# Kernel optimization log

Hardware: AMD Instinct MI355X
Metric: run time of the kernel (lower is better)

## Reference

```python
import jax, jax.numpy as jnp
import numpy as np

N = 100000      # nodes
E = 1600000     # edges (avg degree 16)
B = 64          # graphs in batch
DIN = 128
HID = (256, 128, 64)
EPS = 1e-5


def _gcn(x, W, b, src, dst, n):
    # GCNConv: symmetric normalization with self-loops (already appended to src/dst)
    h = x @ W                                                   # [N, out]
    deg = jax.ops.segment_sum(jnp.ones_like(dst, dtype=h.dtype), dst, num_segments=n)
    dinv = jnp.where(deg > 0, jax.lax.rsqrt(jnp.maximum(deg, 1.0)), 0.0)
    norm = dinv[src] * dinv[dst]                                # [E+N]
    msg = h[src] * norm[:, None]                                # gather + scale
    return jax.ops.segment_sum(msg, dst, num_segments=n) + b    # scatter-add


def _bn(x, g, b):
    # BatchNorm1d over nodes (batch statistics, deterministic)
    mu = x.mean(0)
    var = x.var(0)
    return (x - mu) * jax.lax.rsqrt(var + EPS) * g + b


def setup_inputs():
    key = jax.random.key(0)
    ks = jax.random.split(key, 32)
    inp = {}
    inp["x"] = jax.random.normal(ks[0], (N, DIN), jnp.float32)
    inp["edge_index"] = jax.random.randint(ks[1], (2, E), 0, N, jnp.int32)
    inp["batch"] = jnp.sort(jax.random.randint(ks[2], (N,), 0, B, jnp.int32))
    dims = [DIN] + list(HID)
    for i in range(3):
        inp[f"W{i}"] = jax.random.normal(ks[3 + 4 * i], (dims[i], dims[i + 1]), jnp.float32) / np.sqrt(dims[i]).astype(np.float32)
        inp[f"b{i}"] = jnp.zeros((dims[i + 1],), jnp.float32)
        inp[f"g{i}"] = jnp.ones((dims[i + 1],), jnp.float32)
        inp[f"be{i}"] = jnp.zeros((dims[i + 1],), jnp.float32)
    d = HID[-1]
    inp["ln_g"] = jnp.ones((d,), jnp.float32)
    inp["ln_b"] = jnp.zeros((d,), jnp.float32)
    inp["att"] = jax.random.normal(ks[15], (d, 1), jnp.float32)
    mdims = [d, d // 2, d // 4, 2]
    for i in range(3):
        inp[f"M{i}W"] = jax.random.normal(ks[16 + 2 * i], (mdims[i], mdims[i + 1]), jnp.float32) / np.sqrt(mdims[i]).astype(np.float32)
        inp[f"M{i}b"] = jnp.zeros((mdims[i + 1],), jnp.float32)
    return inp


def reference(x, edge_index, batch, W0, b0, g0, be0, W1, b1, g1, be1, W2, b2, g2, be2,
              ln_g, ln_b, att, M0W, M0b, M1W, M1b, M2W, M2b):
    n = x.shape[0]
    loop = jnp.arange(n, dtype=edge_index.dtype)
    src = jnp.concatenate([edge_index[0], loop])
    dst = jnp.concatenate([edge_index[1], loop])
    for (W, b, g, be) in ((W0, b0, g0, be0), (W1, b1, g1, be1), (W2, b2, g2, be2)):
        x = jax.nn.relu(_bn(_gcn(x, W, b, src, dst, n), g, be))
    # LayerNorm over features
    mu = x.mean(-1, keepdims=True)
    var = x.var(-1, keepdims=True)
    x = (x - mu) * jax.lax.rsqrt(var + EPS) * ln_g + ln_b
    # global attention weights (softmax over ALL nodes, as in original code)
    aw = jax.nn.softmax(jnp.tanh(x @ att), axis=0)   # [N, 1]
    x = x * aw
    # global mean pool per graph
    s = jax.ops.segment_sum(x, batch, num_segments=B)
    cnt = jax.ops.segment_sum(jnp.ones((n, 1), x.dtype), batch, num_segments=B)
    pooled = s / jnp.maximum(cnt, 1.0)               # [B, 64]
    h = jax.nn.relu(pooled @ M0W + M0b)
    h = jax.nn.relu(h @ M1W + M1b)
    return h @ M2W + M2b                             # [B, 2]
```

## Files before the change

### kernel.cpp

```cpp
#include <hip/hip_runtime.h>
#include <hip/hip_bf16.h>
#include <cstdint>
#include <cstddef>

typedef float    f32x4  __attribute__((ext_vector_type(4)));
typedef _Float16 f16x4  __attribute__((ext_vector_type(4)));
typedef _Float16 f16x8  __attribute__((ext_vector_type(8)));

#define BN_G1 1024

__global__ void k_hist(const int* __restrict__ dst, int* __restrict__ deg, int E,
                       unsigned long long M,
                       const int* __restrict__ batch, int* __restrict__ cnt, int n){
  __shared__ int h[64];
  if(threadIdx.x<64) h[threadIdx.x]=0;
  __syncthreads();
  int f   = blockIdx.x & 7;
  int cid = blockIdx.x >> 3;
  int nch = gridDim.x >> 3;
  for(int i = cid*blockDim.x + threadIdx.x; i < E; i += nch*blockDim.x){
    int d = dst[i];
    int xf = (int)(((unsigned long long)(unsigned)d * M) >> 40);
    if(xf == f) atomicAdd(&deg[d], 1);
  }
  for(int i = blockIdx.x*blockDim.x + threadIdx.x; i < n; i += gridDim.x*blockDim.x)
    atomicAdd(&h[batch[i]], 1);
  __syncthreads();
  if(threadIdx.x<64 && h[threadIdx.x]) atomicAdd(&cnt[threadIdx.x], h[threadIdx.x]);
}

__global__ void k_scan1(const int* __restrict__ deg, int* __restrict__ bsum, int n){
  __shared__ int s[256];
  int base = blockIdx.x*1024 + threadIdx.x*4;
  int acc=0;
  #pragma unroll
  for(int j=0;j<4;j++){ int i=base+j; if(i<n) acc+=deg[i]; }
  s[threadIdx.x]=acc; __syncthreads();
  for(int off=128;off>0;off>>=1){
    if(threadIdx.x<off) s[threadIdx.x]+=s[threadIdx.x+off];
    __syncthreads();
  }
  if(threadIdx.x==0) bsum[blockIdx.x]=s[0];
}

__global__ void k_scan2(int* __restrict__ bsum, int nblk, int* __restrict__ rowptr, int n){
  __shared__ int s[128];
  int t=threadIdx.x;
  int v = (t<nblk)? bsum[t] : 0;
  s[t]=v; __syncthreads();
  for(int off=1; off<128; off<<=1){
    int a = (t>=off)? s[t-off] : 0;
    __syncthreads();
    s[t]+=a;
    __syncthreads();
  }
  if(t<nblk) bsum[t]=s[t]-v;
  if(t==127) rowptr[n]=s[127];
}

__global__ void k_scan3(const int* __restrict__ deg, const int* __restrict__ bsum,
                        int* __restrict__ rowptr, int* __restrict__ cursor, int n){
  __shared__ int s[256];
  int base = blockIdx.x*1024 + threadIdx.x*4;
  int v[4]; int acc=0;
  #pragma unroll
  for(int j=0;j<4;j++){ int i=base+j; v[j]=(i<n)?deg[i]:0; acc+=v[j]; }
  s[threadIdx.x]=acc; __syncthreads();
  for(int off=1; off<256; off<<=1){
    int a = (threadIdx.x>=off)? s[threadIdx.x-off] : 0;
    __syncthreads();
    s[threadIdx.x]+=a;
    __syncthreads();
  }
  int excl = s[threadIdx.x]-acc + bsum[blockIdx.x];
  #pragma unroll
  for(int j=0;j<4;j++){
    int i=base+j;
    if(i<n){ rowptr[i]=excl; cursor[i]=excl; excl+=v[j]; }
  }
}

__global__ void k_csr_fill(const int* __restrict__ src, const int* __restrict__ dst,
                           int* __restrict__ cursor, int* __restrict__ adj, int E,
                           unsigned long long M){
  int f   = blockIdx.x & 7;
  int cid = blockIdx.x >> 3;
  int nch = gridDim.x >> 3;
  for(int i = cid*blockDim.x + threadIdx.x; i < E; i += nch*blockDim.x){
    int d = dst[i];
    int xf = (int)(((unsigned long long)(unsigned)d * M) >> 40);
    if(xf == f){
      int p = atomicAdd(&cursor[d], 1);
      adj[p] = src[i];
    }
  }
}


__global__ void k_prep_w3(const float* __restrict__ W0, const float* __restrict__ W1,
                          const float* __restrict__ W2,
                          _Float16* __restrict__ Wh0, _Float16* __restrict__ Wl0,
                          _Float16* __restrict__ Wh1, _Float16* __restrict__ Wl1,
                          _Float16* __restrict__ Wh2, _Float16* __restrict__ Wl2){
  int i = blockIdx.x*256 + threadIdx.x;
  const float* W; _Float16 *Wh, *Wl; int K, F, idx;
  if(i < 32768){        W=W0; Wh=Wh0; Wl=Wl0; K=128; F=256; idx=i; }
  else if(i < 65536){   W=W1; Wh=Wh1; Wl=Wl1; K=256; F=128; idx=i-32768; }
  else if(i < 73728){   W=W2; Wh=Wh2; Wl=Wl2; K=128; F=64;  idx=i-65536; }
  else return;
  int k = idx / F, f = idx % F;
  float a = W[idx];
  _Float16 h = (_Float16)a;
  Wh[(size_t)f*K + k] = h;
  Wl[(size_t)f*K + k] = (_Float16)(a - (float)h);
}

__global__ void k_prep_x(const float* __restrict__ x, const int* __restrict__ deg,
                         float* __restrict__ dinv, _Float16* __restrict__ x16, int n){
  int tid = blockIdx.x*256 + threadIdx.x;
  int node = tid >> 5;
  if(node>=n) return;
  int c4 = tid & 31;
  float d = rsqrtf((float)(deg[node]+1));
  if(c4==0) dinv[node] = d;
  size_t idx = ((size_t)node<<5) + c4;
  float4 v = ((const float4*)x)[idx];
  f16x4 o;
  o[0]=(_Float16)(v.x*d); o[1]=(_Float16)(v.y*d); o[2]=(_Float16)(v.z*d); o[3]=(_Float16)(v.w*d);
  ((f16x4*)x16)[idx] = o;
}

__global__ void k_agg16(const _Float16* __restrict__ zs, const int* __restrict__ rowptr,
                        const int* __restrict__ adj, const float* __restrict__ dinv,
                        const float* __restrict__ bias, _Float16* __restrict__ out,
                        int n, int lg8){
  int tid = blockIdx.x*blockDim.x + threadIdx.x;
  int node = tid >> lg8;
  if(node>=n) return;
  int c8 = tid & ((1<<lg8)-1);
  const f16x8* z8 = (const f16x8*)zs;
  size_t rb = ((size_t)node<<lg8) + c8;
  f16x8 self = z8[rb];
  float a0[8], a1[8], a2[8], a3[8];
  #pragma unroll
  for(int j=0;j<8;j++){ a0[j]=(float)self[j]; a1[j]=0.f; a2[j]=0.f; a3[j]=0.f; }
  int e = rowptr[node], end = rowptr[node+1];
  for(; e+3<end; e+=4){
    int s0=adj[e], s1=adj[e+1], s2=adj[e+2], s3=adj[e+3];
    f16x8 v0 = z8[((size_t)s0<<lg8)+c8];
    f16x8 v1 = z8[((size_t)s1<<lg8)+c8];
    f16x8 v2 = z8[((size_t)s2<<lg8)+c8];
    f16x8 v3 = z8[((size_t)s3<<lg8)+c8];
    #pragma unroll
    for(int j=0;j<8;j++){
      a0[j]+=(float)v0[j]; a1[j]+=(float)v1[j];
      a2[j]+=(float)v2[j]; a3[j]+=(float)v3[j];
    }
  }
  for(; e<end; e++){
    f16x8 v0 = z8[((size_t)adj[e]<<lg8)+c8];
    #pragma unroll
    for(int j=0;j<8;j++) a0[j]+=(float)v0[j];
  }
  float di = dinv[node];
  f16x8 o;
  #pragma unroll
  for(int j=0;j<8;j++){
    float r = ((a0[j]+a1[j])+(a2[j]+a3[j]))*di;
    if(bias) r += bias[(c8<<3)+j];
    o[j] = (_Float16)r;
  }
  ((f16x8*)out)[rb] = o;
}

template<int K, int F, bool BN, bool BIAS, bool RSC>
__global__ __launch_bounds__(256,2) void k_gemm_mfma(const _Float16* __restrict__ A,
    const _Float16* __restrict__ Bh, const _Float16* __restrict__ Bl,
    const float* __restrict__ sc, const float* __restrict__ sh,
    const float* __restrict__ bias, const float* __restrict__ rsc,
    _Float16* __restrict__ C, int n){
  constexpr int NF = F/16;
  __shared__ uint4 sBh[F*4];
  __shared__ uint4 sBl[F*4];
  const int l   = threadIdx.x & 63;
  const int w   = threadIdx.x >> 6;
  const int rlo = l & 15;
  const int khi = l >> 4;
  const int row0 = blockIdx.x*128 + w*32;

  f32x4 acc[2][NF];
  #pragma unroll
  for(int i=0;i<2;i++)
    #pragma unroll
    for(int j=0;j<NF;j++) acc[i][j] = (f32x4){0.f,0.f,0.f,0.f};

  const size_t e0 = (size_t)min(row0 + rlo,      n-1) * K + khi*8;
  const size_t e1 = (size_t)min(row0 + 16 + rlo, n-1) * K + khi*8;

  f16x8 c0 = *(const f16x8*)(A + e0);
  f16x8 c1 = *(const f16x8*)(A + e1);
  f16x8 n0v, n1v;

  #pragma unroll 1
  for(int k0=0; k0<K; k0+=32){
    if(k0+32 < K){
      n0v = *(const f16x8*)(A + e0 + k0 + 32);
      n1v = *(const f16x8*)(A + e1 + k0 + 32);
    }
    __syncthreads();
    #pragma unroll
    for(int j=0;j<F/64;j++){
      int i  = threadIdx.x + j*256;
      int f  = i >> 2;
      int k8 = i & 3;
      int g  = ((f>>4)<<6) + (k8<<4) + (f&15);
      size_t goff = (size_t)f*K + k0 + (k8<<3);
      sBh[g] = *(const uint4*)(Bh + goff);
      sBl[g] = *(const uint4*)(Bl + goff);
    }
    f16x8 a0, a1;
    if(BN){
      float scr[8], shr[8];
      float4 s0 = *(const float4*)(sc + k0 + khi*8);
      float4 s1 = *(const float4*)(sc + k0 + khi*8 + 4);
      float4 t0 = *(const float4*)(sh + k0 + khi*8);
      float4 t1 = *(const float4*)(sh + k0 + khi*8 + 4);
      scr[0]=s0.x;scr[1]=s0.y;scr[2]=s0.z;scr[3]=s0.w;scr[4]=s1.x;scr[5]=s1.y;scr[6]=s1.z;scr[7]=s1.w;
      shr[0]=t0.x;shr[1]=t0.y;shr[2]=t0.z;shr[3]=t0.w;shr[4]=t1.x;shr[5]=t1.y;shr[6]=t1.z;shr[7]=t1.w;
      #pragma unroll
      for(int j=0;j<8;j++){
        a0[j] = (_Float16)fmaxf(fmaf((float)c0[j],scr[j],shr[j]),0.f);
        a1[j] = (_Float16)fmaxf(fmaf((float)c1[j],scr[j],shr[j]),0.f);
      }
    }else{
      a0 = c0; a1 = c1;
    }
    __syncthreads();
    #pragma unroll
    for(int cf=0; cf<NF; cf++){
      f16x8 bh = ((const f16x8*)sBh)[cf*64 + l];
      f16x8 bl = ((const f16x8*)sBl)[cf*64 + l];
      acc[0][cf] = __builtin_amdgcn_mfma_f32_16x16x32_f16(a0, bh, acc[0][cf], 0,0,0);
      acc[1][cf] = __builtin_amdgcn_mfma_f32_16x16x32_f16(a1, bh, acc[1][cf], 0,0,0);
      acc[0][cf] = __builtin_amdgcn_mfma_f32_16x16x32_f16(a0, bl, acc[0][cf], 0,0,0);
      acc[1][cf] = __builtin_amdgcn_mfma_f32_16x16x32_f16(a1, bl, acc[1][cf], 0,0,0);
    }
    c0=n0v; c1=n1v;
  }

  #pragma unroll
  for(int rf=0; rf<2; rf++){
    #pragma unroll
    for(int r=0; r<4; r++){
      int m = row0 + rf*16 + khi*4 + r;
      if(m < n){
        float rs = RSC ? rsc[m] : 1.f;
        #pragma unroll
        for(int cf=0; cf<NF; cf++){
          int col = rlo + 16*cf;
          float v = acc[rf][cf][r];
          if(BIAS) v += bias[col];
          v *= rs;
          C[(size_t)m*F + col] = (_Float16)v;
        }
      }
    }
  }
}

__global__ __launch_bounds__(256) void k_bn_stats16(const _Float16* __restrict__ h,
                            float* __restrict__ partials, int n, int lgF){
  const int F   = 1 << lgF;
  const int C8  = 1 << (lgF-3);
  const int c8  = threadIdx.x & (C8-1);
  const int sub = threadIdx.x >> (lgF-3);
  const int rpb = 256 >> (lgF-3);
  float s[8], s2[8];
  #pragma unroll
  for(int j=0;j<8;j++){ s[j]=0.f; s2[j]=0.f; }
  for(int row = blockIdx.x*rpb + sub; row < n; row += gridDim.x*rpb){
    f16x8 v = ((const f16x8*)h)[(size_t)row*C8 + c8];
    #pragma unroll
    for(int j=0;j<8;j++){ float f=(float)v[j]; s[j]+=f; s2[j]=fmaf(f,f,s2[j]); }
  }
  __shared__ float rs [256*9];
  __shared__ float rs2[256*9];
  #pragma unroll
  for(int j=0;j<8;j++){ rs[threadIdx.x*9+j]=s[j]; rs2[threadIdx.x*9+j]=s2[j]; }
  __syncthreads();
  for(int half = rpb>>1; half>=1; half>>=1){
    if(sub < half){
      int o = (threadIdx.x + half*C8)*9;
      #pragma unroll
      for(int j=0;j<8;j++){ rs[threadIdx.x*9+j]+=rs[o+j]; rs2[threadIdx.x*9+j]+=rs2[o+j]; }
    }
    __syncthreads();
  }
  if(sub==0){
    float* p = partials + (size_t)blockIdx.x*(2*F);
    #pragma unroll
    for(int j=0;j<8;j++){
      p[c8*8+j]     = rs [threadIdx.x*9+j];
      p[F + c8*8+j] = rs2[threadIdx.x*9+j];
    }
  }
}

__global__ void k_bn_fin2(const float* __restrict__ partials, int F,
                          const float* __restrict__ g, const float* __restrict__ be,
                          float* __restrict__ scale, float* __restrict__ shift, int n){
  int c = blockIdx.x*64 + threadIdx.x;
  float s=0.f, s2=0.f;
  #pragma unroll 8
  for(int b=0; b<BN_G1; b++){
    const float* p = partials + (size_t)b*2*F;
    s  += p[c];
    s2 += p[F + c];
  }
  float mu = s/(float)n;
  float var = s2/(float)n - mu*mu;
  float sc = g[c]*rsqrtf(var+1e-5f);
  scale[c] = sc;
  shift[c] = fmaf(-mu, sc, be[c]);
}

__global__ void k_ln_att(const _Float16* __restrict__ x, const float* __restrict__ bsc, const float* __restrict__ bsh,
                         const float* __restrict__ g, const float* __restrict__ b,
                         const float* __restrict__ att, float* __restrict__ lnx, float* __restrict__ wv,
                         float* __restrict__ Ssum, int n){
  int lane = threadIdx.x & 63;
  int wid = (blockIdx.x<<2) + (threadIdx.x>>6);
  float gl=g[lane], bl=b[lane], al=att[lane];
  float scl=bsc[lane], shl=bsh[lane];
  float wacc=0.f;
  for(int node=wid; node<n; node+=4096){
    float raw = (float)x[((size_t)node<<6)+lane];
    float v = fmaxf(fmaf(raw, scl, shl), 0.f);
    float s=v;
    #pragma unroll
    for(int o=32;o>0;o>>=1) s += __shfl_xor(s,o);
    float mu = s*0.015625f;
    float d = v-mu;
    float q = d*d;
    #pragma unroll
    for(int o=32;o>0;o>>=1) q += __shfl_xor(q,o);
    float ln = d*rsqrtf(q*0.015625f + 1e-5f)*gl + bl;
    lnx[((size_t)node<<6)+lane] = ln;
    float a = ln*al;
    #pragma unroll
    for(int o=32;o>0;o>>=1) a += __shfl_xor(a,o);
    float wgt = expf(tanhf(a));
    if(lane==0) wv[node]=wgt;
    wacc += wgt;
  }
  __shared__ float sred[4];
  if(lane==0) sred[threadIdx.x>>6]=wacc;
  __syncthreads();
  if(threadIdx.x==0) atomicAdd(Ssum, sred[0]+sred[1]+sred[2]+sred[3]);
}

__global__ void k_pool(const float* __restrict__ lnx, const float* __restrict__ wv,
                       const int* __restrict__ batch, float* __restrict__ psum, int n){
  int lane = threadIdx.x & 63;
  int wave = threadIdx.x >> 6;
  int start = blockIdx.x*512 + wave*128;
  if(start >= n) return;
  int end = min(start+128, n);
  int cur = batch[start];
  float acc = 0.f;
  for(int i=start;i<end;i++){
    int bb = batch[i];
    if(bb != cur){ atomicAdd(&psum[cur*64+lane], acc); acc=0.f; cur=bb; }
    acc = fmaf(lnx[(size_t)i*64+lane], wv[i], acc);
  }
  atomicAdd(&psum[cur*64+lane], acc);
}

__global__ void k_mlp(const float* __restrict__ psum, const int* __restrict__ cnt,
                      const float* __restrict__ Ssum,
                      const float* __restrict__ M0W, const float* __restrict__ M0b,
                      const float* __restrict__ M1W, const float* __restrict__ M1b,
                      const float* __restrict__ M2W, const float* __restrict__ M2b,
                      float* __restrict__ out){
  int b = threadIdx.x;
  float S = Ssum[0];
  int cb = cnt[b]; if(cb<1) cb=1;
  float inv = 1.f/(S*(float)cb);
  float p[64];
  #pragma unroll
  for(int f=0;f<64;f++) p[f] = psum[b*64+f]*inv;
  float h1[32];
  #pragma unroll
  for(int j=0;j<32;j++){
    float a=M0b[j];
    #pragma unroll
    for(int f=0;f<64;f++) a = fmaf(p[f], M0W[f*32+j], a);
    h1[j]=fmaxf(a,0.f);
  }
  float h2[16];
  #pragma unroll
  for(int j=0;j<16;j++){
    float a=M1b[j];
    #pragma unroll
    for(int f=0;f<32;f++) a = fmaf(h1[f], M1W[f*16+j], a);
    h2[j]=fmaxf(a,0.f);
  }
  #pragma unroll
  for(int j=0;j<2;j++){
    float a=M2b[j];
    #pragma unroll
    for(int f=0;f<16;f++) a = fmaf(h2[f], M2W[f*2+j], a);
    out[b*2+j]=a;
  }
}


extern "C" void kernel_launch(void* const* d_in, const int* in_sizes, int n_in,
                              void* d_out, int out_size, void* d_ws, size_t ws_size,
                              hipStream_t stream){
  const float* x   = (const float*)d_in[0];
  const int*   ei  = (const int*)d_in[1];
  const int* batch = (const int*)d_in[2];
  const float* W0=(const float*)d_in[3],  *b0=(const float*)d_in[4],  *g0=(const float*)d_in[5],  *be0=(const float*)d_in[6];
  const float* W1=(const float*)d_in[7],  *b1=(const float*)d_in[8],  *g1=(const float*)d_in[9],  *be1=(const float*)d_in[10];
  const float* W2=(const float*)d_in[11], *b2=(const float*)d_in[12], *g2=(const float*)d_in[13], *be2=(const float*)d_in[14];
  const float* ln_g=(const float*)d_in[15], *ln_b=(const float*)d_in[16], *att=(const float*)d_in[17];
  const float* M0W=(const float*)d_in[18], *M0b=(const float*)d_in[19];
  const float* M1W=(const float*)d_in[20], *M1b=(const float*)d_in[21];
  const float* M2W=(const float*)d_in[22], *M2b=(const float*)d_in[23];
  const int N = in_sizes[0]/128;
  const int E = in_sizes[1]/2;
  const int* srcv = ei;
  const int* dstv = ei + E;
  const unsigned long long Mdiv = ((8ULL<<40) + (unsigned long long)N - 1) / (unsigned long long)N;

  char* base = (char*)d_ws;
  size_t off = 0;
  auto alloc = [&](size_t bytes)->char*{ char* p = base+off; off = (off+bytes+255)&~(size_t)255; return p; };
  int*   deg    = (int*)  alloc((size_t)N*4);
  int*   cnt    = (int*)  alloc(64*4);
  float* psum   = (float*)alloc(64*64*4);
  float* Ssum   = (float*)alloc(4);
  size_t zero_bytes = off;
  float* dinv   = (float*)alloc((size_t)N*4);
  int*   rowptr = (int*)  alloc(((size_t)N+1)*4);
  int*   cursor = (int*)  alloc((size_t)N*4);
  int*   bsum   = (int*)  alloc(128*4);
  float* bnsc   = (float*)alloc(3*256*4);
  float* bnsh   = (float*)alloc(3*256*4);
  float* partials = (float*)alloc((size_t)BN_G1*512*4);
  _Float16* Wh0 = (_Float16*)alloc((size_t)128*256*2);
  _Float16* Wl0 = (_Float16*)alloc((size_t)128*256*2);
  _Float16* Wh1 = (_Float16*)alloc((size_t)256*128*2);
  _Float16* Wl1 = (_Float16*)alloc((size_t)256*128*2);
  _Float16* Wh2 = (_Float16*)alloc((size_t)128*64*2);
  _Float16* Wl2 = (_Float16*)alloc((size_t)128*64*2);
  int*   adj    = (int*)  alloc((size_t)E*4);
  _Float16* x16 = (_Float16*)alloc((size_t)N*128*2);
  _Float16* R16 = (_Float16*)alloc((size_t)N*128*2);
  _Float16* P16 = (_Float16*)alloc((size_t)N*256*2);
  _Float16* Q16 = (_Float16*)alloc((size_t)N*128*2);
  _Float16* O16 = (_Float16*)alloc((size_t)N*64*2);
  float* LNX    = (float*)alloc((size_t)N*64*4);
  float* WV     = (float*)alloc((size_t)N*4);
  (void)ws_size; (void)n_in; (void)out_size;

  hipMemsetAsync(d_ws, 0, zero_bytes, stream);

  k_hist <<<2048,256,0,stream>>>(dstv, deg, E, Mdiv, batch, cnt, N);
  int nblk = (N+1023)/1024;
  k_scan1<<<nblk,256,0,stream>>>(deg, bsum, N);
  k_scan2<<<1,128,0,stream>>>(bsum, nblk, rowptr, N);
  k_scan3<<<nblk,256,0,stream>>>(deg, bsum, rowptr, cursor, N);
  k_csr_fill<<<2048,256,0,stream>>>(srcv, dstv, cursor, adj, E, Mdiv);
  k_prep_w3<<<288,256,0,stream>>>(W0,W1,W2, Wh0,Wl0, Wh1,Wl1, Wh2,Wl2);
  k_prep_x<<<(N*32+255)/256,256,0,stream>>>(x, deg, dinv, x16, N);

  const int gemm_grid = (N+127)/128;

  k_agg16<<<(N*16+255)/256,256,0,stream>>>(x16, rowptr, adj, dinv, nullptr, R16, N, 4);
  k_gemm_mfma<128,256,false,true,false><<<gemm_grid,256,0,stream>>>(R16, Wh0, Wl0, nullptr,nullptr, b0, nullptr, P16, N);
  k_bn_stats16<<<BN_G1,256,0,stream>>>(P16, partials, N, 8);
  k_bn_fin2<<<4,64,0,stream>>>(partials, 256, g0, be0, bnsc+0, bnsh+0, N);

  k_gemm_mfma<256,128,true,false,true><<<gemm_grid,256,0,stream>>>(P16, Wh1, Wl1, bnsc+0, bnsh+0, nullptr, dinv, Q16, N);
  k_agg16<<<(N*16+255)/256,256,0,stream>>>(Q16, rowptr, adj, dinv, b1, R16, N, 4);
  k_bn_stats16<<<BN_G1,256,0,stream>>>(R16, partials, N, 7);
  k_bn_fin2<<<2,64,0,stream>>>(partials, 128, g1, be1, bnsc+256, bnsh+256, N);

  k_gemm_mfma<128,64,true,false,true><<<gemm_grid,256,0,stream>>>(R16, Wh2, Wl2, bnsc+256, bnsh+256, nullptr, dinv, Q16, N);
  k_agg16<<<(N*8+255)/256,256,0,stream>>>(Q16, rowptr, adj, dinv, b2, O16, N, 3);
  k_bn_stats16<<<BN_G1,256,0,stream>>>(O16, partials, N, 6);
  k_bn_fin2<<<1,64,0,stream>>>(partials, 64, g2, be2, bnsc+512, bnsh+512, N);

  k_ln_att<<<1024,256,0,stream>>>(O16, bnsc+512, bnsh+512, ln_g, ln_b, att, LNX, WV, Ssum, N);
  k_pool  <<<(N+511)/512,256,0,stream>>>(LNX, WV, batch, psum, N);
  k_mlp   <<<1,64,0,stream>>>(psum, cnt, Ssum, M0W,M0b,M1W,M1b,M2W,M2b, (float*)d_out);
}
```

Measured before the change: 685.0 us.

## Fuse BatchNorm statistics into GEMM/aggregation epilogues and store LN output as fp16

Removes the standalone BN-stats kernels by computing per-column sum and sum-of-squares in the epilogues of the first GEMM and the second and third aggregation kernels. The per-block partials are then reduced in two levels (colsum slices, then finalize). This avoids rereading each large activation tensor just for statistics. It also stores the LayerNorm output in fp16 to halve pool traffic, and computes the attention weight with a clamped exp2-based tanh/exp. The costs are extra shared-memory reductions and barriers in the producer kernels, one extra small launch per layer, and slightly lower precision in the pooled features.

```diff
diff --git a/kernel.cpp b/kernel.cpp
--- a/kernel.cpp
+++ b/kernel.cpp
@@ -6,8 +6,6 @@
 typedef float    f32x4  __attribute__((ext_vector_type(4)));
 typedef _Float16 f16x4  __attribute__((ext_vector_type(4)));
 typedef _Float16 f16x8  __attribute__((ext_vector_type(8)));
-
-#define BN_G1 1024
 
 __global__ void k_hist(const int* __restrict__ dst, int* __restrict__ deg, int E,
                        unsigned long long M,
@@ -95,7 +93,6 @@
     }
   }
 }
-
 
 __global__ void k_prep_w3(const float* __restrict__ W0, const float* __restrict__ W1,
                           const float* __restrict__ W2,
@@ -130,55 +127,94 @@
   ((f16x4*)x16)[idx] = o;
 }
 
+template<bool STATS>
 __global__ void k_agg16(const _Float16* __restrict__ zs, const int* __restrict__ rowptr,
                         const int* __restrict__ adj, const float* __restrict__ dinv,
                         const float* __restrict__ bias, _Float16* __restrict__ out,
-                        int n, int lg8){
+                        float* __restrict__ partials, int n, int lg8){
   int tid = blockIdx.x*blockDim.x + threadIdx.x;
   int node = tid >> lg8;
-  if(node>=n) return;
-  int c8 = tid & ((1<<lg8)-1);
-  const f16x8* z8 = (const f16x8*)zs;
-  size_t rb = ((size_t)node<<lg8) + c8;
-  f16x8 self = z8[rb];
-  float a0[8], a1[8], a2[8], a3[8];
-  #pragma unroll
-  for(int j=0;j<8;j++){ a0[j]=(float)self[j]; a1[j]=0.f; a2[j]=0.f; a3[j]=0.f; }
-  int e = rowptr[node], end = rowptr[node+1];
-  for(; e+3<end; e+=4){
-    int s0=adj[e], s1=adj[e+1], s2=adj[e+2], s3=adj[e+3];
-    f16x8 v0 = z8[((size_t)s0<<lg8)+c8];
-    f16x8 v1 = z8[((size_t)s1<<lg8)+c8];
-    f16x8 v2 = z8[((size_t)s2<<lg8)+c8];
-    f16x8 v3 = z8[((size_t)s3<<lg8)+c8];
+  const int C8 = 1<<lg8;
+  int c8 = threadIdx.x & (C8-1);
+  bool valid = node < n;
+  if(!STATS && !valid) return;
+  float rr[8];
+  #pragma unroll
+  for(int j=0;j<8;j++) rr[j]=0.f;
+  if(valid){
+    const f16x8* z8 = (const f16x8*)zs;
+    size_t rb = ((size_t)node<<lg8) + c8;
+    f16x8 self = z8[rb];
+    float a0[8], a1[8], a2[8], a3[8];
+    #pragma unroll
+    for(int j=0;j<8;j++){ a0[j]=(float)self[j]; a1[j]=0.f; a2[j]=0.f; a3[j]=0.f; }
+    int e = rowptr[node], end = rowptr[node+1];
+    for(; e+3<end; e+=4){
+      int s0=adj[e], s1=adj[e+1], s2=adj[e+2], s3=adj[e+3];
+      f16x8 v0 = z8[((size_t)s0<<lg8)+c8];
+      f16x8 v1 = z8[((size_t)s1<<lg8)+c8];
+      f16x8 v2 = z8[((size_t)s2<<lg8)+c8];
+      f16x8 v3 = z8[((size_t)s3<<lg8)+c8];
+      #pragma unroll
+      for(int j=0;j<8;j++){
+        a0[j]+=(float)v0[j]; a1[j]+=(float)v1[j];
+        a2[j]+=(float)v2[j]; a3[j]+=(float)v3[j];
+      }
+    }
+    for(; e<end; e++){
+      f16x8 v0 = z8[((size_t)adj[e]<<lg8)+c8];
+      #pragma unroll
+      for(int j=0;j<8;j++) a0[j]+=(float)v0[j];
+    }
+    float di = dinv[node];
+    f16x8 o;
     #pragma unroll
     for(int j=0;j<8;j++){
-      a0[j]+=(float)v0[j]; a1[j]+=(float)v1[j];
-      a2[j]+=(float)v2[j]; a3[j]+=(float)v3[j];
-    }
-  }
-  for(; e<end; e++){
-    f16x8 v0 = z8[((size_t)adj[e]<<lg8)+c8];
-    #pragma unroll
-    for(int j=0;j<8;j++) a0[j]+=(float)v0[j];
-  }
-  float di = dinv[node];
-  f16x8 o;
-  #pragma unroll
-  for(int j=0;j<8;j++){
-    float r = ((a0[j]+a1[j])+(a2[j]+a3[j]))*di;
-    if(bias) r += bias[(c8<<3)+j];
-    o[j] = (_Float16)r;
-  }
-  ((f16x8*)out)[rb] = o;
-}
-
-template<int K, int F, bool BN, bool BIAS, bool RSC>
+      float r = ((a0[j]+a1[j])+(a2[j]+a3[j]))*di;
+      if(bias) r += bias[(c8<<3)+j];
+      rr[j]=r;
+      o[j] = (_Float16)r;
+    }
+    ((f16x8*)out)[rb] = o;
+  }
+  if constexpr(STATS){
+    __shared__ float rs [256*9];
+    __shared__ float rs2[256*9];
+    int sub = threadIdx.x >> lg8;
+    int npb = 256 >> lg8;
+    #pragma unroll
+    for(int j=0;j<8;j++){
+      float v = valid ? rr[j] : 0.f;
+      rs [threadIdx.x*9+j] = v;
+      rs2[threadIdx.x*9+j] = v*v;
+    }
+    __syncthreads();
+    for(int half = npb>>1; half>=1; half>>=1){
+      if(sub < half){
+        int o = (threadIdx.x + half*C8)*9;
+        #pragma unroll
+        for(int j=0;j<8;j++){ rs[threadIdx.x*9+j]+=rs[o+j]; rs2[threadIdx.x*9+j]+=rs2[o+j]; }
+      }
+      __syncthreads();
+    }
+    if(sub==0){
+      int F = 8<<lg8;
+      float* p = partials + (size_t)blockIdx.x*(2*F);
+      #pragma unroll
+      for(int j=0;j<8;j++){
+        p[c8*8+j]     = rs [threadIdx.x*9+j];
+        p[F + c8*8+j] = rs2[threadIdx.x*9+j];
+      }
+    }
+  }
+}
+
+template<int K, int F, bool BN, bool BIAS, bool RSC, bool STATS>
 __global__ __launch_bounds__(256,2) void k_gemm_mfma(const _Float16* __restrict__ A,
     const _Float16* __restrict__ Bh, const _Float16* __restrict__ Bl,
     const float* __restrict__ sc, const float* __restrict__ sh,
     const float* __restrict__ bias, const float* __restrict__ rsc,
-    _Float16* __restrict__ C, int n){
+    _Float16* __restrict__ C, float* __restrict__ partials, int n){
   constexpr int NF = F/16;
   __shared__ uint4 sBh[F*4];
   __shared__ uint4 sBl[F*4];
@@ -248,75 +284,73 @@
     c0=n0v; c1=n1v;
   }
 
+  float ts[NF], ts2[NF];
+  if constexpr(STATS){
+    #pragma unroll
+    for(int cf=0;cf<NF;cf++){ ts[cf]=0.f; ts2[cf]=0.f; }
+  }
   #pragma unroll
   for(int rf=0; rf<2; rf++){
     #pragma unroll
     for(int r=0; r<4; r++){
       int m = row0 + rf*16 + khi*4 + r;
       if(m < n){
-        float rs = RSC ? rsc[m] : 1.f;
+        float rscv = RSC ? rsc[m] : 1.f;
         #pragma unroll
         for(int cf=0; cf<NF; cf++){
           int col = rlo + 16*cf;
           float v = acc[rf][cf][r];
           if(BIAS) v += bias[col];
-          v *= rs;
+          v *= rscv;
           C[(size_t)m*F + col] = (_Float16)v;
+          if constexpr(STATS){ ts[cf]+=v; ts2[cf]=fmaf(v,v,ts2[cf]); }
         }
       }
     }
   }
-}
-
-__global__ __launch_bounds__(256) void k_bn_stats16(const _Float16* __restrict__ h,
-                            float* __restrict__ partials, int n, int lgF){
-  const int F   = 1 << lgF;
-  const int C8  = 1 << (lgF-3);
-  const int c8  = threadIdx.x & (C8-1);
-  const int sub = threadIdx.x >> (lgF-3);
-  const int rpb = 256 >> (lgF-3);
-  float s[8], s2[8];
-  #pragma unroll
-  for(int j=0;j<8;j++){ s[j]=0.f; s2[j]=0.f; }
-  for(int row = blockIdx.x*rpb + sub; row < n; row += gridDim.x*rpb){
-    f16x8 v = ((const f16x8*)h)[(size_t)row*C8 + c8];
-    #pragma unroll
-    for(int j=0;j<8;j++){ float f=(float)v[j]; s[j]+=f; s2[j]=fmaf(f,f,s2[j]); }
-  }
-  __shared__ float rs [256*9];
-  __shared__ float rs2[256*9];
-  #pragma unroll
-  for(int j=0;j<8;j++){ rs[threadIdx.x*9+j]=s[j]; rs2[threadIdx.x*9+j]=s2[j]; }
-  __syncthreads();
-  for(int half = rpb>>1; half>=1; half>>=1){
-    if(sub < half){
-      int o = (threadIdx.x + half*C8)*9;
+  if constexpr(STATS){
+    __shared__ float sstat[4][16][NF][2];
+    #pragma unroll
+    for(int cf=0;cf<NF;cf++){
+      ts [cf] += __shfl_xor(ts [cf],16); ts [cf] += __shfl_xor(ts [cf],32);
+      ts2[cf] += __shfl_xor(ts2[cf],16); ts2[cf] += __shfl_xor(ts2[cf],32);
+    }
+    if(khi==0){
       #pragma unroll
-      for(int j=0;j<8;j++){ rs[threadIdx.x*9+j]+=rs[o+j]; rs2[threadIdx.x*9+j]+=rs2[o+j]; }
-    }
-    __syncthreads();
-  }
-  if(sub==0){
-    float* p = partials + (size_t)blockIdx.x*(2*F);
-    #pragma unroll
-    for(int j=0;j<8;j++){
-      p[c8*8+j]     = rs [threadIdx.x*9+j];
-      p[F + c8*8+j] = rs2[threadIdx.x*9+j];
-    }
-  }
-}
-
-__global__ void k_bn_fin2(const float* __restrict__ partials, int F,
+      for(int cf=0;cf<NF;cf++){ sstat[w][rlo][cf][0]=ts[cf]; sstat[w][rlo][cf][1]=ts2[cf]; }
+    }
+    __syncthreads();
+    {
+      int rl = threadIdx.x & 15, cf = threadIdx.x >> 4;
+      float s_=0.f, s2_=0.f;
+      #pragma unroll
+      for(int ww=0; ww<4; ww++){ s_+=sstat[ww][rl][cf][0]; s2_+=sstat[ww][rl][cf][1]; }
+      int col = rl + 16*cf;
+      partials[(size_t)blockIdx.x*(2*F) + col]     = s_;
+      partials[(size_t)blockIdx.x*(2*F) + F + col] = s2_;
+    }
+  }
+}
+
+__global__ void k_colsum1(const float* __restrict__ partials, float* __restrict__ lvl1,
+                          int F2, int nblk){
+  int c = blockIdx.x*64 + threadIdx.x;
+  int slice = blockIdx.y;
+  int b0 = (int)(((long long)nblk *  slice   ) >> 6);
+  int b1 = (int)(((long long)nblk * (slice+1)) >> 6);
+  float s = 0.f;
+  for(int b=b0; b<b1; b++) s += partials[(size_t)b*F2 + c];
+  lvl1[slice*F2 + c] = s;
+}
+
+__global__ void k_bn_fin2(const float* __restrict__ lvl1, int F,
                           const float* __restrict__ g, const float* __restrict__ be,
                           float* __restrict__ scale, float* __restrict__ shift, int n){
   int c = blockIdx.x*64 + threadIdx.x;
+  int F2 = 2*F;
   float s=0.f, s2=0.f;
-  #pragma unroll 8
-  for(int b=0; b<BN_G1; b++){
-    const float* p = partials + (size_t)b*2*F;
-    s  += p[c];
-    s2 += p[F + c];
-  }
+  #pragma unroll
+  for(int k=0;k<64;k++){ s += lvl1[k*F2 + c]; s2 += lvl1[k*F2 + F + c]; }
   float mu = s/(float)n;
   float var = s2/(float)n - mu*mu;
   float sc = g[c]*rsqrtf(var+1e-5f);
@@ -324,34 +358,62 @@
   shift[c] = fmaf(-mu, sc, be[c]);
 }
 
+__device__ __forceinline__ float attw(float a){
+  float t = fminf(fmaxf(a,-15.f),15.f);
+  float u = exp2f(t*2.885390082f);
+  float th = (u-1.f)/(u+1.f);
+  return exp2f(th*1.442695041f);
+}
+
 __global__ void k_ln_att(const _Float16* __restrict__ x, const float* __restrict__ bsc, const float* __restrict__ bsh,
                          const float* __restrict__ g, const float* __restrict__ b,
-                         const float* __restrict__ att, float* __restrict__ lnx, float* __restrict__ wv,
+                         const float* __restrict__ att, _Float16* __restrict__ lnx, float* __restrict__ wv,
                          float* __restrict__ Ssum, int n){
   int lane = threadIdx.x & 63;
   int wid = (blockIdx.x<<2) + (threadIdx.x>>6);
   float gl=g[lane], bl=b[lane], al=att[lane];
   float scl=bsc[lane], shl=bsh[lane];
   float wacc=0.f;
-  for(int node=wid; node<n; node+=4096){
-    float raw = (float)x[((size_t)node<<6)+lane];
-    float v = fmaxf(fmaf(raw, scl, shl), 0.f);
-    float s=v;
-    #pragma unroll
-    for(int o=32;o>0;o>>=1) s += __shfl_xor(s,o);
-    float mu = s*0.015625f;
-    float d = v-mu;
-    float q = d*d;
-    #pragma unroll
-    for(int o=32;o>0;o>>=1) q += __shfl_xor(q,o);
-    float ln = d*rsqrtf(q*0.015625f + 1e-5f)*gl + bl;
-    lnx[((size_t)node<<6)+lane] = ln;
-    float a = ln*al;
-    #pragma unroll
-    for(int o=32;o>0;o>>=1) a += __shfl_xor(a,o);
-    float wgt = expf(tanhf(a));
-    if(lane==0) wv[node]=wgt;
-    wacc += wgt;
+  int node = wid;
+  for(; node+4096 < n; node += 8192){
+    int n1 = node + 4096;
+    float v0 = fmaxf(fmaf((float)x[((size_t)node<<6)+lane], scl, shl), 0.f);
+    float v1 = fmaxf(fmaf((float)x[((size_t)n1  <<6)+lane], scl, shl), 0.f);
+    float s0=v0, s1=v1;
+    #pragma unroll
+    for(int o=32;o>0;o>>=1){ s0+=__shfl_xor(s0,o); s1+=__shfl_xor(s1,o); }
+    float d0=v0-s0*0.015625f, d1=v1-s1*0.015625f;
+    float q0=d0*d0, q1=d1*d1;
+    #pragma unroll
+    for(int o=32;o>0;o>>=1){ q0+=__shfl_xor(q0,o); q1+=__shfl_xor(q1,o); }
+    float ln0 = d0*rsqrtf(q0*0.015625f+1e-5f)*gl+bl;
+    float ln1 = d1*rsqrtf(q1*0.015625f+1e-5f)*gl+bl;
+    lnx[((size_t)node<<6)+lane]=(_Float16)ln0;
+    lnx[((size_t)n1  <<6)+lane]=(_Float16)ln1;
+    float a0=ln0*al, a1=ln1*al;
+    #pragma unroll
+    for(int o=32;o>0;o>>=1){ a0+=__shfl_xor(a0,o); a1+=__shfl_xor(a1,o); }
+    float w0=attw(a0), w1=attw(a1);
+    if(lane==0){ wv[node]=w0; wv[n1]=w1; }
+    wacc += w0+w1;
+  }
+  for(; node<n; node+=4096){
+    float v0 = fmaxf(fmaf((float)x[((size_t)node<<6)+lane], scl, shl), 0.f);
+    float s0=v0;
+    #pragma unroll
+    for(int o=32;o>0;o>>=1) s0+=__shfl_xor(s0,o);
+    float d0=v0-s0*0.015625f;
+    float q0=d0*d0;
+    #pragma unroll
+    for(int o=32;o>0;o>>=1) q0+=__shfl_xor(q0,o);
+    float ln0 = d0*rsqrtf(q0*0.015625f+1e-5f)*gl+bl;
+    lnx[((size_t)node<<6)+lane]=(_Float16)ln0;
+    float a0=ln0*al;
+    #pragma unroll
+    for(int o=32;o>0;o>>=1) a0+=__shfl_xor(a0,o);
+    float w0=attw(a0);
+    if(lane==0) wv[node]=w0;
+    wacc += w0;
   }
   __shared__ float sred[4];
   if(lane==0) sred[threadIdx.x>>6]=wacc;
@@ -359,7 +421,7 @@
   if(threadIdx.x==0) atomicAdd(Ssum, sred[0]+sred[1]+sred[2]+sred[3]);
 }
 
-__global__ void k_pool(const float* __restrict__ lnx, const float* __restrict__ wv,
+__global__ void k_pool(const _Float16* __restrict__ lnx, const float* __restrict__ wv,
                        const int* __restrict__ batch, float* __restrict__ psum, int n){
   int lane = threadIdx.x & 63;
   int wave = threadIdx.x >> 6;
@@ -371,7 +433,7 @@
   for(int i=start;i<end;i++){
     int bb = batch[i];
     if(bb != cur){ atomicAdd(&psum[cur*64+lane], acc); acc=0.f; cur=bb; }
-    acc = fmaf(lnx[(size_t)i*64+lane], wv[i], acc);
+    acc = fmaf((float)lnx[(size_t)i*64+lane], wv[i], acc);
   }
   atomicAdd(&psum[cur*64+lane], acc);
 }
@@ -434,6 +496,10 @@
   const int* dstv = ei + E;
   const unsigned long long Mdiv = ((8ULL<<40) + (unsigned long long)N - 1) / (unsigned long long)N;
 
+  const int gemm_grid = (N+127)/128;
+  const int agg_grid1 = (N*16+255)/256;
+  const int agg_grid2 = (N*8+255)/256;
+
   char* base = (char*)d_ws;
   size_t off = 0;
   auto alloc = [&](size_t bytes)->char*{ char* p = base+off; off = (off+bytes+255)&~(size_t)255; return p; };
@@ -448,7 +514,8 @@
   int*   bsum   = (int*)  alloc(128*4);
   float* bnsc   = (float*)alloc(3*256*4);
   float* bnsh   = (float*)alloc(3*256*4);
-  float* partials = (float*)alloc((size_t)BN_G1*512*4);
+  float* partials = (float*)alloc((size_t)agg_grid1*256*4);
+  float* lvl1   = (float*)alloc((size_t)64*512*4);
   _Float16* Wh0 = (_Float16*)alloc((size_t)128*256*2);
   _Float16* Wl0 = (_Float16*)alloc((size_t)128*256*2);
   _Float16* Wh1 = (_Float16*)alloc((size_t)256*128*2);
@@ -461,7 +528,7 @@
   _Float16* P16 = (_Float16*)alloc((size_t)N*256*2);
   _Float16* Q16 = (_Float16*)alloc((size_t)N*128*2);
   _Float16* O16 = (_Float16*)alloc((size_t)N*64*2);
-  float* LNX    = (float*)alloc((size_t)N*64*4);
+  _Float16* LNX = (_Float16*)alloc((size_t)N*64*2);
   float* WV     = (float*)alloc((size_t)N*4);
   (void)ws_size; (void)n_in; (void)out_size;
 
@@ -476,22 +543,20 @@
   k_prep_w3<<<288,256,0,stream>>>(W0,W1,W2, Wh0,Wl0, Wh1,Wl1, Wh2,Wl2);
   k_prep_x<<<(N*32+255)/256,256,0,stream>>>(x, deg, dinv, x16, N);
 
-  const int gemm_grid = (N+127)/128;
-
-  k_agg16<<<(N*16+255)/256,256,0,stream>>>(x16, rowptr, adj, dinv, nullptr, R16, N, 4);
-  k_gemm_mfma<128,256,false,true,false><<<gemm_grid,256,0,stream>>>(R16, Wh0, Wl0, nullptr,nullptr, b0, nullptr, P16, N);
-  k_bn_stats16<<<BN_G1,256,0,stream>>>(P16, partials, N, 8);
-  k_bn_fin2<<<4,64,0,stream>>>(partials, 256, g0, be0, bnsc+0, bnsh+0, N);
-
-  k_gemm_mfma<256,128,true,false,true><<<gemm_grid,256,0,stream>>>(P16, Wh1, Wl1, bnsc+0, bnsh+0, nullptr, dinv, Q16, N);
-  k_agg16<<<(N*16+255)/256,256,0,stream>>>(Q16, rowptr, adj, dinv, b1, R16, N, 4);
-  k_bn_stats16<<<BN_G1,256,0,stream>>>(R16, partials, N, 7);
-  k_bn_fin2<<<2,64,0,stream>>>(partials, 128, g1, be1, bnsc+256, bnsh+256, N);
-
-  k_gemm_mfma<128,64,true,false,true><<<gemm_grid,256,0,stream>>>(R16, Wh2, Wl2, bnsc+256, bnsh+256, nullptr, dinv, Q16, N);
-  k_agg16<<<(N*8+255)/256,256,0,stream>>>(Q16, rowptr, adj, dinv, b2, O16, N, 3);
-  k_bn_stats16<<<BN_G1,256,0,stream>>>(O16, partials, N, 6);
-  k_bn_fin2<<<1,64,0,stream>>>(partials, 64, g2, be2, bnsc+512, bnsh+512, N);
+  k_agg16<false><<<agg_grid1,256,0,stream>>>(x16, rowptr, adj, dinv, nullptr, R16, nullptr, N, 4);
+  k_gemm_mfma<128,256,false,true,false,true><<<gemm_grid,256,0,stream>>>(R16, Wh0, Wl0, nullptr,nullptr, b0, nullptr, P16, partials, N);
+  k_colsum1<<<dim3(8,64),64,0,stream>>>(partials, lvl1, 512, gemm_grid);
+  k_bn_fin2<<<4,64,0,stream>>>(lvl1, 256, g0, be0, bnsc+0, bnsh+0, N);
+
+  k_gemm_mfma<256,128,true,false,true,false><<<gemm_grid,256,0,stream>>>(P16, Wh1, Wl1, bnsc+0, bnsh+0, nullptr, dinv, Q16, nullptr, N);
+  k_agg16<true><<<agg_grid1,256,0,stream>>>(Q16, rowptr, adj, dinv, b1, R16, partials, N, 4);
+  k_colsum1<<<dim3(4,64),64,0,stream>>>(partials, lvl1, 256, agg_grid1);
+  k_bn_fin2<<<2,64,0,stream>>>(lvl1, 128, g1, be1, bnsc+256, bnsh+256, N);
+
+  k_gemm_mfma<128,64,true,false,true,false><<<gemm_grid,256,0,stream>>>(R16, Wh2, Wl2, bnsc+256, bnsh+256, nullptr, dinv, Q16, nullptr, N);
+  k_agg16<true><<<agg_grid2,256,0,stream>>>(Q16, rowptr, adj, dinv, b2, O16, partials, N, 3);
+  k_colsum1<<<dim3(2,64),64,0,stream>>>(partials, lvl1, 128, agg_grid2);
+  k_bn_fin2<<<1,64,0,stream>>>(lvl1, 64, g2, be2, bnsc+512, bnsh+512, N);
 
   k_ln_att<<<1024,256,0,stream>>>(O16, bnsc+512, bnsh+512, ln_g, ln_b, att, LNX, WV, Ssum, N);
   k_pool  <<<(N+511)/512,256,0,stream>>>(LNX, WV, batch, psum, N);
```

After: 596.1 us. 1.15x faster.
